# Performance work log

Hardware: AMD Instinct MI355X
Metric: run time of the kernel (lower is better)

Reference implementation:

```python
import jax, jax.numpy as jnp
import numpy as np

N, E, G = 50000, 400000, 512
F_IN, H = 128, 128  # OPS_LENGTH, hidden_channels
NEG_SLOPE = 0.2
BN_EPS = 1e-5


def seg_softmax(e, idx, n):
    m = jax.ops.segment_max(e, idx, num_segments=n)
    ex = jnp.exp(e - m[idx])
    s = jax.ops.segment_sum(ex, idx, num_segments=n)
    return ex / (s[idx] + 1e-16)


def gatv2(x, src, dst, Wl, Wr, att, b, n):
    # PyG GATv2Conv, heads=1: e = att . leaky_relu(Wl x_src + Wr x_dst),
    # alpha = softmax over incoming edges per dst, out = sum alpha * Wl x_src + b
    xl = x @ Wl
    xr = x @ Wr
    z = jax.nn.leaky_relu(xl[src] + xr[dst], NEG_SLOPE)  # [E, out]
    e = jnp.einsum('ed,d->e', z, att)
    a = seg_softmax(e, dst, n)
    return jax.ops.segment_sum(xl[src] * a[:, None], dst, num_segments=n) + b


def bn_eval(x, g, b, m, v):
    return (x - m) * jax.lax.rsqrt(v + BN_EPS) * g + b


def setup_inputs() -> dict:
    key = jax.random.key(0)
    ks = jax.random.split(key, 40)
    d = {}
    d['x'] = jax.random.normal(ks[0], (N, F_IN), dtype=jnp.float32)
    d['edge_index'] = jax.random.randint(ks[1], (2, E), 0, N)
    d['batch'] = jnp.sort(jax.random.randint(ks[2], (N,), 0, G))
    def lin(k, i, o, s=None):
        s = s if s is not None else 1.0 / np.sqrt(i)
        return jax.random.normal(k, (i, o), dtype=jnp.float32) * s
    # conv1: 128->128, conv2: 128->256, conv3: 256->128
    d['Wl1'] = lin(ks[3], F_IN, H); d['Wr1'] = lin(ks[4], F_IN, H)
    d['att1'] = jax.random.normal(ks[5], (H,), dtype=jnp.float32) * 0.1
    d['b1'] = jnp.zeros((H,), jnp.float32)
    d['Wl2'] = lin(ks[6], H, 2 * H); d['Wr2'] = lin(ks[7], H, 2 * H)
    d['att2'] = jax.random.normal(ks[8], (2 * H,), dtype=jnp.float32) * 0.1
    d['b2'] = jnp.zeros((2 * H,), jnp.float32)
    d['Wl3'] = lin(ks[9], 2 * H, H); d['Wr3'] = lin(ks[10], 2 * H, H)
    d['att3'] = jax.random.normal(ks[11], (H,), dtype=jnp.float32) * 0.1
    d['b3'] = jnp.zeros((H,), jnp.float32)
    d['Wlin1'] = lin(ks[12], H, 128); d['blin1'] = jnp.zeros((128,), jnp.float32)
    d['Wlin2'] = lin(ks[13], 128, 64); d['blin2'] = jnp.zeros((64,), jnp.float32)
    d['Wlin3'] = lin(ks[14], 64, 2); d['blin3'] = jnp.zeros((2,), jnp.float32)
    for name, dim, i in [('bng', H, 15), ('bn1', 128, 19), ('bn2', 64, 23)]:
        d[name + '_g'] = jax.random.uniform(ks[i], (dim,), minval=0.5, maxval=1.5)
        d[name + '_b'] = jax.random.normal(ks[i + 1], (dim,), dtype=jnp.float32) * 0.1
        d[name + '_m'] = jax.random.normal(ks[i + 2], (dim,), dtype=jnp.float32) * 0.1
        d[name + '_v'] = jax.random.uniform(ks[i + 3], (dim,), minval=0.5, maxval=1.5)
    return d


def reference(x, edge_index, batch, Wl1, Wr1, att1, b1, Wl2, Wr2, att2, b2,
              Wl3, Wr3, att3, b3, Wlin1, blin1, Wlin2, blin2, Wlin3, blin3,
              bng_g, bng_b, bng_m, bng_v, bn1_g, bn1_b, bn1_m, bn1_v,
              bn2_g, bn2_b, bn2_m, bn2_v):
    src, dst = edge_index[0], edge_index[1]
    h = jax.nn.relu(gatv2(x, src, dst, Wl1, Wr1, att1, b1, N))
    h = jax.nn.relu(gatv2(h, src, dst, Wl2, Wr2, att2, b2, N))
    h = gatv2(h, src, dst, Wl3, Wr3, att3, b3, N)
    # global_mean_pool
    sums = jax.ops.segment_sum(h, batch, num_segments=G)
    cnt = jax.ops.segment_sum(jnp.ones((N,), h.dtype), batch, num_segments=G)
    g = sums / jnp.maximum(cnt, 1.0)[:, None]
    # dropout p=0.5 is identity in eval mode; BatchNorms in eval mode
    g = bn_eval(g, bng_g, bng_b, bng_m, bng_v)
    g = bn_eval(jax.nn.relu(g @ Wlin1 + blin1), bn1_g, bn1_b, bn1_m, bn1_v)
    g = bn_eval(jax.nn.relu(g @ Wlin2 + blin2), bn2_g, bn2_b, bn2_m, bn2_v)
    return jax.nn.relu(g @ Wlin3 + blin3)
```

## Files before the change

### kernel.cpp

```cpp
#include <hip/hip_runtime.h>
#include <math.h>

#define N_NODES 50000
#define N_EDGES 400000
#define N_GRAPHS 512
#define NEG_SLOPE 0.2f
#define BN_EPS 1e-5f
#define SCAN_BLOCKS 49

#define C6 0.8656170245333781f
#define C4 0.5770780163555854f
#define THR_LOG2 11.541560327111708f

typedef __attribute__((ext_vector_type(8))) short bf16x8;
typedef __attribute__((ext_vector_type(4))) float f32x4;

__device__ __forceinline__ ushort f2b(float f) {
    unsigned u = __float_as_uint(f);
    unsigned r = (u + 0x7fffu + ((u >> 16) & 1u)) >> 16;
    return (ushort)r;
}
__device__ __forceinline__ float b2f(ushort u) {
    return __uint_as_float((unsigned)u << 16);
}

__global__ void cvt_kernel(const float* __restrict__ in, ushort* __restrict__ out,
                           int total4) {
    const int i = blockIdx.x * 256 + threadIdx.x;
    if (i >= total4) return;
    float4 v = *(const float4*)(in + (size_t)i * 4);
    ushort4 o;
    o.x = f2b(v.x); o.y = f2b(v.y); o.z = f2b(v.z); o.w = f2b(v.w);
    *(ushort4*)(out + (size_t)i * 4) = o;
}

__global__ void wcvt_all_kernel(const float* __restrict__ Wl1, const float* __restrict__ Wr1,
                                const float* __restrict__ Wl2, const float* __restrict__ Wr2,
                                const float* __restrict__ Wl3, const float* __restrict__ Wr3,
                                ushort* __restrict__ wt1, ushort* __restrict__ wt2,
                                ushort* __restrict__ wt3) {
    const int i = blockIdx.x * 256 + threadIdx.x;
    if (i < 32768) {
        const int m = i >> 7, k = i & 127;
        const float v = (m < 128) ? Wl1[k * 128 + m] : Wr1[k * 128 + (m - 128)];
        wt1[i] = f2b(v);
    } else if (i < 98304) {
        const int j = i - 32768;
        const int m = j >> 7, k = j & 127;
        const float v = (m < 256) ? Wl2[k * 256 + m] : Wr2[k * 256 + (m - 256)];
        wt2[j] = f2b(v);
    } else if (i < 163840) {
        const int j = i - 98304;
        const int m = j >> 8, k = j & 255;
        const float v = (m < 128) ? Wl3[k * 128 + m] : Wr3[k * 128 + (m - 128)];
        wt3[j] = f2b(v);
    }
}

__global__ __launch_bounds__(256) void gemm_bf16_kernel(
    const ushort* __restrict__ A, const ushort* __restrict__ Bt,
    ushort* __restrict__ Cl, float* __restrict__ Cr, int n, int K, int FO) {
    __shared__ ushort As[128][40];
    __shared__ ushort Bs[128][40];
    const int tid = threadIdx.x;
    const int row0 = blockIdx.x * 128;
    const int col0 = blockIdx.y * 128;
    const int w = tid >> 6, lane = tid & 63;
    const int wr = (w >> 1) * 64, wc = (w & 1) * 64;
    const int lr = lane & 15, kg = lane >> 4;

    const int srow = tid >> 1, shalf = tid & 1;

    f32x4 acc[4][4];
#pragma unroll
    for (int i = 0; i < 4; ++i)
#pragma unroll
        for (int j = 0; j < 4; ++j) acc[i][j] = (f32x4){0.f, 0.f, 0.f, 0.f};

    for (int k0 = 0; k0 < K; k0 += 32) {
        {
            const int gr = row0 + srow;
            uint4 v0 = make_uint4(0, 0, 0, 0), v1 = v0;
            if (gr < n) {
                const uint4* p = (const uint4*)(A + (size_t)gr * K + k0) + shalf * 2;
                v0 = p[0]; v1 = p[1];
            }
            uint4* d = (uint4*)&As[srow][shalf * 16];
            d[0] = v0; d[1] = v1;
            const int gb = col0 + srow;
            const uint4* p = (const uint4*)(Bt + (size_t)gb * K + k0) + shalf * 2;
            uint4* db = (uint4*)&Bs[srow][shalf * 16];
            db[0] = p[0]; db[1] = p[1];
        }
        __syncthreads();
        bf16x8 af[4], bfr[4];
#pragma unroll
        for (int mi = 0; mi < 4; ++mi)
            af[mi] = *(const bf16x8*)&As[wr + mi * 16 + lr][kg * 8];
#pragma unroll
        for (int ni = 0; ni < 4; ++ni)
            bfr[ni] = *(const bf16x8*)&Bs[wc + ni * 16 + lr][kg * 8];
#pragma unroll
        for (int mi = 0; mi < 4; ++mi)
#pragma unroll
            for (int ni = 0; ni < 4; ++ni)
                acc[mi][ni] = __builtin_amdgcn_mfma_f32_16x16x32_bf16(
                    af[mi], bfr[ni], acc[mi][ni], 0, 0, 0);
        __syncthreads();
    }
    const bool left = (col0 < FO);
    const int cbase = left ? col0 : col0 - FO;
#pragma unroll
    for (int mi = 0; mi < 4; ++mi)
#pragma unroll
        for (int ni = 0; ni < 4; ++ni)
#pragma unroll
            for (int j = 0; j < 4; ++j) {
                const int r = row0 + wr + mi * 16 + kg * 4 + j;
                if (r < n) {
                    const int c = cbase + wc + ni * 16 + lr;
                    if (left)
                        Cl[(size_t)r * FO + c] = f2b(acc[mi][ni][j]);
                    else
                        Cr[(size_t)r * FO + c] = acc[mi][ni][j];
                }
            }
}

__global__ void deg_count_kernel(const int* __restrict__ ei, int* __restrict__ deg) {
    const int e = blockIdx.x * 256 + threadIdx.x;
    if (e < N_EDGES) atomicAdd(&deg[ei[N_EDGES + e]], 1);
}

__global__ __launch_bounds__(256) void scanA_kernel(const int* __restrict__ deg,
                                                    int* __restrict__ rowp,
                                                    int* __restrict__ bsum) {
    const int t = threadIdx.x, b = blockIdx.x;
    const int i0 = b * 1024 + t * 4;
    int4 d = make_int4(0, 0, 0, 0);
    if (i0 + 3 < N_NODES) d = *(const int4*)(deg + i0);
    else {
        if (i0 + 0 < N_NODES) d.x = deg[i0 + 0];
        if (i0 + 1 < N_NODES) d.y = deg[i0 + 1];
        if (i0 + 2 < N_NODES) d.z = deg[i0 + 2];
    }
    const int tsum = d.x + d.y + d.z + d.w;
    int inc = tsum;
    const int lane = t & 63, wave = t >> 6;
#pragma unroll
    for (int o = 1; o < 64; o <<= 1) {
        int v = __shfl_up(inc, o, 64);
        if (lane >= o) inc += v;
    }
    __shared__ int wsum[4];
    if (lane == 63) wsum[wave] = inc;
    __syncthreads();
    int wbase = 0;
#pragma unroll
    for (int ww = 0; ww < 4; ++ww)
        if (ww < wave) wbase += wsum[ww];
    const int texcl = wbase + inc - tsum;
    int4 o4;
    o4.x = texcl;
    o4.y = o4.x + d.x;
    o4.z = o4.y + d.y;
    o4.w = o4.z + d.z;
    if (i0 + 3 < N_NODES) *(int4*)(rowp + i0) = o4;
    else {
        if (i0 + 0 < N_NODES) rowp[i0 + 0] = o4.x;
        if (i0 + 1 < N_NODES) rowp[i0 + 1] = o4.y;
        if (i0 + 2 < N_NODES) rowp[i0 + 2] = o4.z;
    }
    if (t == 255) bsum[b] = wbase + inc;
}

__global__ __launch_bounds__(256) void scanC_kernel(const int* __restrict__ bsum,
                                                    int* __restrict__ rowp) {
    const int t = threadIdx.x, b = blockIdx.x;
    __shared__ int base_s;
    if (t < 64) {
        int v = (t < b) ? bsum[t] : 0;
#pragma unroll
        for (int o = 32; o; o >>= 1) v += __shfl_xor(v, o, 64);
        if (t == 0) base_s = v;
    }
    __syncthreads();
    const int base = base_s;
    const int i0 = b * 1024 + t * 4;
    if (base != 0) {
        if (i0 + 3 < N_NODES) {
            int4 v = *(int4*)(rowp + i0);
            v.x += base; v.y += base; v.z += base; v.w += base;
            *(int4*)(rowp + i0) = v;
        } else {
            if (i0 + 0 < N_NODES) rowp[i0 + 0] += base;
            if (i0 + 1 < N_NODES) rowp[i0 + 1] += base;
            if (i0 + 2 < N_NODES) rowp[i0 + 2] += base;
        }
    }
    if (b == 0 && t == 0) rowp[N_NODES] = N_EDGES;
}

__global__ void csr_fill_kernel(const int* __restrict__ ei, const int* __restrict__ rowp,
                                int* __restrict__ cursor, int* __restrict__ csr_src) {
    const int e = blockIdx.x * 256 + threadIdx.x;
    if (e >= N_EDGES) return;
    const int d = ei[N_EDGES + e];
    const int pos = atomicAdd(&cursor[d], 1);
    csr_src[rowp[d] + pos] = ei[e];
}

template <int VEC>
__device__ __forceinline__ void sm_upd(float& m, float& s, float* acc, float p,
                                       const float* l) {
    if (p > m + THR_LOG2) {
        const float sc = __builtin_amdgcn_exp2f(m - p);
        s = s * sc + 1.f;
#pragma unroll
        for (int k = 0; k < VEC; ++k) acc[k] = acc[k] * sc + l[k];
        m = p;
    } else {
        const float w = __builtin_amdgcn_exp2f(p - m);
        s += w;
#pragma unroll
        for (int k = 0; k < VEC; ++k) acc[k] += w * l[k];
    }
}

template <int FO, int VEC>
__global__ __launch_bounds__(256) void gat_edge_kernel(
    const int* __restrict__ rowp, const int* __restrict__ csr_src,
    const ushort* __restrict__ xlb, const float* __restrict__ xr,
    const float* __restrict__ att, const float* __restrict__ bias,
    float* __restrict__ outf, ushort* __restrict__ outb, int do_relu) {
    const int d = blockIdx.x * 4 + (threadIdx.x >> 6);
    const int lane = threadIdx.x & 63;
    if (d >= N_NODES) return;
    const int co = lane * VEC;

    float a6[VEC], a4[VEC], r[VEC];
    if constexpr (VEC == 4) {
        float4 t4 = *(const float4*)(att + co);
        a6[0] = C6 * t4.x; a6[1] = C6 * t4.y; a6[2] = C6 * t4.z; a6[3] = C6 * t4.w;
        a4[0] = C4 * t4.x; a4[1] = C4 * t4.y; a4[2] = C4 * t4.z; a4[3] = C4 * t4.w;
        t4 = *(const float4*)(xr + (size_t)d * FO + co);
        r[0] = t4.x; r[1] = t4.y; r[2] = t4.z; r[3] = t4.w;
    } else {
        float2 t2 = *(const float2*)(att + co);
        a6[0] = C6 * t2.x; a6[1] = C6 * t2.y;
        a4[0] = C4 * t2.x; a4[1] = C4 * t2.y;
        t2 = *(const float2*)(xr + (size_t)d * FO + co);
        r[0] = t2.x; r[1] = t2.y;
    }

    const int jb = rowp[d], je = rowp[d + 1];
    float m0 = -INFINITY, s0 = 0.f, m1 = -INFINITY, s1 = 0.f;
    float acc0[VEC] = {}, acc1[VEC] = {};

    int j = jb;
    for (; j + 1 < je; j += 2) {
        const int src0 = csr_src[j];
        const int src1 = csr_src[j + 1];
        float l0[VEC], l1[VEC];
        if constexpr (VEC == 4) {
            ushort4 t0 = *(const ushort4*)(xlb + (size_t)src0 * FO + co);
            ushort4 t1 = *(const ushort4*)(xlb + (size_t)src1 * FO + co);
            l0[0] = b2f(t0.x); l0[1] = b2f(t0.y); l0[2] = b2f(t0.z); l0[3] = b2f(t0.w);
            l1[0] = b2f(t1.x); l1[1] = b2f(t1.y); l1[2] = b2f(t1.z); l1[3] = b2f(t1.w);
        } else {
            ushort2 t0 = *(const ushort2*)(xlb + (size_t)src0 * FO + co);
            ushort2 t1 = *(const ushort2*)(xlb + (size_t)src1 * FO + co);
            l0[0] = b2f(t0.x); l0[1] = b2f(t0.y);
            l1[0] = b2f(t1.x); l1[1] = b2f(t1.y);
        }
        float p0 = 0.f, p1 = 0.f;
#pragma unroll
        for (int k = 0; k < VEC; ++k) {
            const float z0 = l0[k] + r[k];
            const float z1 = l1[k] + r[k];
            p0 = fmaf(a6[k], z0, p0); p0 = fmaf(a4[k], fabsf(z0), p0);
            p1 = fmaf(a6[k], z1, p1); p1 = fmaf(a4[k], fabsf(z1), p1);
        }
#pragma unroll
        for (int o = 32; o; o >>= 1) {
            p0 += __shfl_xor(p0, o, 64);
            p1 += __shfl_xor(p1, o, 64);
        }
        sm_upd<VEC>(m0, s0, acc0, p0, l0);
        sm_upd<VEC>(m1, s1, acc1, p1, l1);
    }
    if (j < je) {
        const int src0 = csr_src[j];
        float l0[VEC];
        if constexpr (VEC == 4) {
            ushort4 t0 = *(const ushort4*)(xlb + (size_t)src0 * FO + co);
            l0[0] = b2f(t0.x); l0[1] = b2f(t0.y); l0[2] = b2f(t0.z); l0[3] = b2f(t0.w);
        } else {
            ushort2 t0 = *(const ushort2*)(xlb + (size_t)src0 * FO + co);
            l0[0] = b2f(t0.x); l0[1] = b2f(t0.y);
        }
        float p0 = 0.f;
#pragma unroll
        for (int k = 0; k < VEC; ++k) {
            const float z0 = l0[k] + r[k];
            p0 = fmaf(a6[k], z0, p0); p0 = fmaf(a4[k], fabsf(z0), p0);
        }
#pragma unroll
        for (int o = 32; o; o >>= 1) p0 += __shfl_xor(p0, o, 64);
        sm_upd<VEC>(m0, s0, acc0, p0, l0);
    }

    float s, acc[VEC];
    if (je > jb) {
        const float M = fmaxf(m0, m1);
        const float sc0 = __builtin_amdgcn_exp2f(m0 - M);
        const float sc1 = __builtin_amdgcn_exp2f(m1 - M);
        s = s0 * sc0 + s1 * sc1;
#pragma unroll
        for (int k = 0; k < VEC; ++k) acc[k] = acc0[k] * sc0 + acc1[k] * sc1;
    } else {
        s = 0.f;
#pragma unroll
        for (int k = 0; k < VEC; ++k) acc[k] = 0.f;
    }

    const float inv = 1.f / (s + 1e-16f);
#pragma unroll
    for (int k = 0; k < VEC; ++k) {
        float v = acc[k] * inv + bias[co + k];
        if (do_relu) v = fmaxf(v, 0.f);
        acc[k] = v;
    }
    if (outf) {
        if constexpr (VEC == 4)
            *(float4*)(outf + (size_t)d * FO + co) = make_float4(acc[0], acc[1], acc[2], acc[3]);
        else
            *(float2*)(outf + (size_t)d * FO + co) = make_float2(acc[0], acc[1]);
    }
    if (outb) {
        if constexpr (VEC == 4) {
            ushort4 o; o.x = f2b(acc[0]); o.y = f2b(acc[1]); o.z = f2b(acc[2]); o.w = f2b(acc[3]);
            *(ushort4*)(outb + (size_t)d * FO + co) = o;
        } else {
            ushort2 o; o.x = f2b(acc[0]); o.y = f2b(acc[1]);
            *(ushort2*)(outb + (size_t)d * FO + co) = o;
        }
    }
}

__global__ void gstart_kernel(const int* __restrict__ batch, int* __restrict__ gstart) {
    const int i = blockIdx.x * 256 + threadIdx.x;
    if (i >= N_NODES) return;
    const int b = batch[i];
    if (i == 0) {
        for (int g = 0; g <= b; ++g) gstart[g] = 0;
    } else {
        const int pb = batch[i - 1];
        for (int g = pb + 1; g <= b; ++g) gstart[g] = i;
    }
    if (i == N_NODES - 1) {
        for (int g = b + 1; g <= N_GRAPHS; ++g) gstart[g] = N_NODES;
    }
}

__global__ __launch_bounds__(128) void pool2_kernel(const float* __restrict__ h,
                                                    const int* __restrict__ gstart,
                                                    float* __restrict__ gsum,
                                                    float* __restrict__ gcnt) {
    const int g = blockIdx.x, t = threadIdx.x;
    const int b = gstart[g], e = gstart[g + 1];
    float s = 0.f;
    for (int i = b; i < e; ++i) s += h[(size_t)i * 128 + t];
    gsum[g * 128 + t] = s;
    if (t == 0) gcnt[g] = (float)(e - b);
}

__global__ __launch_bounds__(128) void mlp_kernel(
    const float* __restrict__ gsum, const float* __restrict__ gcnt,
    const float* __restrict__ W1, const float* __restrict__ b1,
    const float* __restrict__ W2, const float* __restrict__ b2,
    const float* __restrict__ W3, const float* __restrict__ b3,
    const float* __restrict__ bng_g, const float* __restrict__ bng_b,
    const float* __restrict__ bng_m, const float* __restrict__ bng_v,
    const float* __restrict__ bn1_g, const float* __restrict__ bn1_b,
    const float* __restrict__ bn1_m, const float* __restrict__ bn1_v,
    const float* __restrict__ bn2_g, const float* __restrict__ bn2_b,
    const float* __restrict__ bn2_m, const float* __restrict__ bn2_v,
    float* __restrict__ out) {
    __shared__ float s0[128], s1[128], s2[64];
    const int g = blockIdx.x, t = threadIdx.x;
    const float cnt = fmaxf(gcnt[g], 1.f);
    float v = gsum[g * 128 + t] / cnt;
    v = (v - bng_m[t]) * rsqrtf(bng_v[t] + BN_EPS) * bng_g[t] + bng_b[t];
    s0[t] = v;
    __syncthreads();
    float a1 = b1[t];
    for (int i = 0; i < 128; ++i) a1 += s0[i] * W1[i * 128 + t];
    a1 = fmaxf(a1, 0.f);
    a1 = (a1 - bn1_m[t]) * rsqrtf(bn1_v[t] + BN_EPS) * bn1_g[t] + bn1_b[t];
    s1[t] = a1;
    __syncthreads();
    if (t < 64) {
        float a2 = b2[t];
        for (int i = 0; i < 128; ++i) a2 += s1[i] * W2[i * 64 + t];
        a2 = fmaxf(a2, 0.f);
        a2 = (a2 - bn2_m[t]) * rsqrtf(bn2_v[t] + BN_EPS) * bn2_g[t] + bn2_b[t];
        s2[t] = a2;
    }
    __syncthreads();
    if (t < 2) {
        float a3 = b3[t];
        for (int i = 0; i < 64; ++i) a3 += s2[i] * W3[i * 2 + t];
        out[g * 2 + t] = fmaxf(a3, 0.f);
    }
}

extern "C" void kernel_launch(void* const* d_in, const int* in_sizes, int n_in,
                              void* d_out, int out_size, void* d_ws, size_t ws_size,
                              hipStream_t stream) {
    const float* x = (const float*)d_in[0];
    const int* ei = (const int*)d_in[1];
    const int* batch = (const int*)d_in[2];
    const float* Wl1 = (const float*)d_in[3];
    const float* Wr1 = (const float*)d_in[4];
    const float* att1 = (const float*)d_in[5];
    const float* b1 = (const float*)d_in[6];
    const float* Wl2 = (const float*)d_in[7];
    const float* Wr2 = (const float*)d_in[8];
    const float* att2 = (const float*)d_in[9];
    const float* b2 = (const float*)d_in[10];
    const float* Wl3 = (const float*)d_in[11];
    const float* Wr3 = (const float*)d_in[12];
    const float* att3 = (const float*)d_in[13];
    const float* b3 = (const float*)d_in[14];
    const float* Wlin1 = (const float*)d_in[15];
    const float* blin1 = (const float*)d_in[16];
    const float* Wlin2 = (const float*)d_in[17];
    const float* blin2 = (const float*)d_in[18];
    const float* Wlin3 = (const float*)d_in[19];
    const float* blin3 = (const float*)d_in[20];
    const float* bng_g = (const float*)d_in[21];
    const float* bng_b = (const float*)d_in[22];
    const float* bng_m = (const float*)d_in[23];
    const float* bng_v = (const float*)d_in[24];
    const float* bn1_g = (const float*)d_in[25];
    const float* bn1_b = (const float*)d_in[26];
    const float* bn1_m = (const float*)d_in[27];
    const float* bn1_v = (const float*)d_in[28];
    const float* bn2_g = (const float*)d_in[29];
    const float* bn2_b = (const float*)d_in[30];
    const float* bn2_m = (const float*)d_in[31];
    const float* bn2_v = (const float*)d_in[32];

    float* ws = (float*)d_ws;
    ushort* xlb = (ushort*)ws;
    float* xr = (float*)(xlb + (size_t)N_NODES * 256);
    float* h3 = xr + (size_t)N_NODES * 256;
    ushort* hbf = (ushort*)(h3 + (size_t)N_NODES * 128);
    ushort* wt1 = hbf + (size_t)N_NODES * 256;
    ushort* wt2 = wt1 + 256 * 128;
    ushort* wt3 = wt2 + 512 * 128;
    int* deg = (int*)(wt3 + 256 * 256);
    int* cursor = deg + N_NODES;
    int* rowp = cursor + N_NODES;
    int* csr_src = rowp + N_NODES + 1;
    int* gstart = csr_src + N_EDGES;
    int* bsum = gstart + N_GRAPHS + 1;
    float* gsum = (float*)(bsum + SCAN_BLOCKS);
    float* gcnt = gsum + (size_t)N_GRAPHS * 128;

    const int eb = (N_EDGES + 255) / 256;

    hipMemsetAsync(deg, 0, (size_t)N_NODES * 2 * 4, stream);
    deg_count_kernel<<<eb, 256, 0, stream>>>(ei, deg);
    scanA_kernel<<<SCAN_BLOCKS, 256, 0, stream>>>(deg, rowp, bsum);
    scanC_kernel<<<SCAN_BLOCKS, 256, 0, stream>>>(bsum, rowp);
    csr_fill_kernel<<<eb, 256, 0, stream>>>(ei, rowp, cursor, csr_src);
    gstart_kernel<<<(N_NODES + 255) / 256, 256, 0, stream>>>(batch, gstart);

    wcvt_all_kernel<<<640, 256, 0, stream>>>(Wl1, Wr1, Wl2, Wr2, Wl3, Wr3, wt1, wt2, wt3);
    cvt_kernel<<<(N_NODES * 128 / 4 + 255) / 256, 256, 0, stream>>>(
        x, hbf, N_NODES * 128 / 4);

    const int nb = (N_NODES + 3) / 4;
    const int gx = (N_NODES + 127) / 128;

    gemm_bf16_kernel<<<dim3(gx, 2), 256, 0, stream>>>(hbf, wt1, xlb, xr, N_NODES, 128, 128);
    gat_edge_kernel<128, 2><<<nb, 256, 0, stream>>>(rowp, csr_src, xlb, xr,
                                                    att1, b1, nullptr, hbf, 1);
    gemm_bf16_kernel<<<dim3(gx, 4), 256, 0, stream>>>(hbf, wt2, xlb, xr, N_NODES, 128, 256);
    gat_edge_kernel<256, 4><<<nb, 256, 0, stream>>>(rowp, csr_src, xlb, xr,
                                                    att2, b2, nullptr, hbf, 1);
    gemm_bf16_kernel<<<dim3(gx, 2), 256, 0, stream>>>(hbf, wt3, xlb, xr, N_NODES, 256, 128);
    gat_edge_kernel<128, 2><<<nb, 256, 0, stream>>>(rowp, csr_src, xlb, xr,
                                                    att3, b3, h3, nullptr, 0);

    pool2_kernel<<<N_GRAPHS, 128, 0, stream>>>(h3, gstart, gsum, gcnt);

    mlp_kernel<<<N_GRAPHS, 128, 0, stream>>>(
        gsum, gcnt, Wlin1, blin1, Wlin2, blin2, Wlin3, blin3,
        bng_g, bng_b, bng_m, bng_v, bn1_g, bn1_b, bn1_m, bn1_v,
        bn2_g, bn2_b, bn2_m, bn2_v, (float*)d_out);
}
```

Before: 317.3 us.

## Store xl and xr interleaved in bf16 and unroll edge loop by four

The GEMM now writes one interleaved bf16 buffer in which each row holds the xl half followed by the xr half, replacing the separate bf16 xl and fp32 xr arrays. This halves the bytes written for xr and read per destination node. The GAT edge kernel keeps four independent online-softmax accumulators instead of two, giving four gathers in flight per iteration. The costs are reduced precision of xr, a larger row stride for the gathered xl rows that lowers cache density, and more register pressure from the extra accumulators.

```diff
diff --git a/kernel.cpp b/kernel.cpp
--- a/kernel.cpp
+++ b/kernel.cpp
@@ -59,7 +59,7 @@
 
 __global__ __launch_bounds__(256) void gemm_bf16_kernel(
     const ushort* __restrict__ A, const ushort* __restrict__ Bt,
-    ushort* __restrict__ Cl, float* __restrict__ Cr, int n, int K, int FO) {
+    ushort* __restrict__ C, int n, int K, int M) {
     __shared__ ushort As[128][40];
     __shared__ ushort Bs[128][40];
     const int tid = threadIdx.x;
@@ -108,8 +108,6 @@
                     af[mi], bfr[ni], acc[mi][ni], 0, 0, 0);
         __syncthreads();
     }
-    const bool left = (col0 < FO);
-    const int cbase = left ? col0 : col0 - FO;
 #pragma unroll
     for (int mi = 0; mi < 4; ++mi)
 #pragma unroll
@@ -117,13 +115,8 @@
 #pragma unroll
             for (int j = 0; j < 4; ++j) {
                 const int r = row0 + wr + mi * 16 + kg * 4 + j;
-                if (r < n) {
-                    const int c = cbase + wc + ni * 16 + lr;
-                    if (left)
-                        Cl[(size_t)r * FO + c] = f2b(acc[mi][ni][j]);
-                    else
-                        Cr[(size_t)r * FO + c] = acc[mi][ni][j];
-                }
+                if (r < n)
+                    C[(size_t)r * M + col0 + wc + ni * 16 + lr] = f2b(acc[mi][ni][j]);
             }
 }
 
@@ -230,7 +223,7 @@
 template <int FO, int VEC>
 __global__ __launch_bounds__(256) void gat_edge_kernel(
     const int* __restrict__ rowp, const int* __restrict__ csr_src,
-    const ushort* __restrict__ xlb, const float* __restrict__ xr,
+    const ushort* __restrict__ hx,
     const float* __restrict__ att, const float* __restrict__ bias,
     float* __restrict__ outf, ushort* __restrict__ outb, int do_relu) {
     const int d = blockIdx.x * 4 + (threadIdx.x >> 6);
@@ -243,106 +236,110 @@
         float4 t4 = *(const float4*)(att + co);
         a6[0] = C6 * t4.x; a6[1] = C6 * t4.y; a6[2] = C6 * t4.z; a6[3] = C6 * t4.w;
         a4[0] = C4 * t4.x; a4[1] = C4 * t4.y; a4[2] = C4 * t4.z; a4[3] = C4 * t4.w;
-        t4 = *(const float4*)(xr + (size_t)d * FO + co);
-        r[0] = t4.x; r[1] = t4.y; r[2] = t4.z; r[3] = t4.w;
+        ushort4 u4 = *(const ushort4*)(hx + (size_t)d * (2 * FO) + FO + co);
+        r[0] = b2f(u4.x); r[1] = b2f(u4.y); r[2] = b2f(u4.z); r[3] = b2f(u4.w);
     } else {
         float2 t2 = *(const float2*)(att + co);
         a6[0] = C6 * t2.x; a6[1] = C6 * t2.y;
         a4[0] = C4 * t2.x; a4[1] = C4 * t2.y;
-        t2 = *(const float2*)(xr + (size_t)d * FO + co);
-        r[0] = t2.x; r[1] = t2.y;
+        ushort2 u2 = *(const ushort2*)(hx + (size_t)d * (2 * FO) + FO + co);
+        r[0] = b2f(u2.x); r[1] = b2f(u2.y);
     }
 
     const int jb = rowp[d], je = rowp[d + 1];
-    float m0 = -INFINITY, s0 = 0.f, m1 = -INFINITY, s1 = 0.f;
-    float acc0[VEC] = {}, acc1[VEC] = {};
+    float ms[4] = {-INFINITY, -INFINITY, -INFINITY, -INFINITY};
+    float ss[4] = {0.f, 0.f, 0.f, 0.f};
+    float acc[4][VEC] = {};
 
     int j = jb;
-    for (; j + 1 < je; j += 2) {
-        const int src0 = csr_src[j];
-        const int src1 = csr_src[j + 1];
-        float l0[VEC], l1[VEC];
-        if constexpr (VEC == 4) {
-            ushort4 t0 = *(const ushort4*)(xlb + (size_t)src0 * FO + co);
-            ushort4 t1 = *(const ushort4*)(xlb + (size_t)src1 * FO + co);
-            l0[0] = b2f(t0.x); l0[1] = b2f(t0.y); l0[2] = b2f(t0.z); l0[3] = b2f(t0.w);
-            l1[0] = b2f(t1.x); l1[1] = b2f(t1.y); l1[2] = b2f(t1.z); l1[3] = b2f(t1.w);
-        } else {
-            ushort2 t0 = *(const ushort2*)(xlb + (size_t)src0 * FO + co);
-            ushort2 t1 = *(const ushort2*)(xlb + (size_t)src1 * FO + co);
-            l0[0] = b2f(t0.x); l0[1] = b2f(t0.y);
-            l1[0] = b2f(t1.x); l1[1] = b2f(t1.y);
-        }
-        float p0 = 0.f, p1 = 0.f;
-#pragma unroll
-        for (int k = 0; k < VEC; ++k) {
-            const float z0 = l0[k] + r[k];
-            const float z1 = l1[k] + r[k];
-            p0 = fmaf(a6[k], z0, p0); p0 = fmaf(a4[k], fabsf(z0), p0);
-            p1 = fmaf(a6[k], z1, p1); p1 = fmaf(a4[k], fabsf(z1), p1);
+    for (; j + 3 < je; j += 4) {
+        int src[4];
+#pragma unroll
+        for (int q = 0; q < 4; ++q) src[q] = csr_src[j + q];
+        float l[4][VEC];
+        float p[4] = {0.f, 0.f, 0.f, 0.f};
+#pragma unroll
+        for (int q = 0; q < 4; ++q) {
+            if constexpr (VEC == 4) {
+                ushort4 t = *(const ushort4*)(hx + (size_t)src[q] * (2 * FO) + co);
+                l[q][0] = b2f(t.x); l[q][1] = b2f(t.y); l[q][2] = b2f(t.z); l[q][3] = b2f(t.w);
+            } else {
+                ushort2 t = *(const ushort2*)(hx + (size_t)src[q] * (2 * FO) + co);
+                l[q][0] = b2f(t.x); l[q][1] = b2f(t.y);
+            }
+#pragma unroll
+            for (int k = 0; k < VEC; ++k) {
+                const float z = l[q][k] + r[k];
+                p[q] = fmaf(a6[k], z, p[q]);
+                p[q] = fmaf(a4[k], fabsf(z), p[q]);
+            }
         }
 #pragma unroll
         for (int o = 32; o; o >>= 1) {
-            p0 += __shfl_xor(p0, o, 64);
-            p1 += __shfl_xor(p1, o, 64);
-        }
-        sm_upd<VEC>(m0, s0, acc0, p0, l0);
-        sm_upd<VEC>(m1, s1, acc1, p1, l1);
-    }
-    if (j < je) {
+#pragma unroll
+            for (int q = 0; q < 4; ++q) p[q] += __shfl_xor(p[q], o, 64);
+        }
+#pragma unroll
+        for (int q = 0; q < 4; ++q) sm_upd<VEC>(ms[q], ss[q], acc[q], p[q], l[q]);
+    }
+    for (int q = 0; j < je; ++j, ++q) {
         const int src0 = csr_src[j];
         float l0[VEC];
         if constexpr (VEC == 4) {
-            ushort4 t0 = *(const ushort4*)(xlb + (size_t)src0 * FO + co);
-            l0[0] = b2f(t0.x); l0[1] = b2f(t0.y); l0[2] = b2f(t0.z); l0[3] = b2f(t0.w);
+            ushort4 t = *(const ushort4*)(hx + (size_t)src0 * (2 * FO) + co);
+            l0[0] = b2f(t.x); l0[1] = b2f(t.y); l0[2] = b2f(t.z); l0[3] = b2f(t.w);
         } else {
-            ushort2 t0 = *(const ushort2*)(xlb + (size_t)src0 * FO + co);
-            l0[0] = b2f(t0.x); l0[1] = b2f(t0.y);
+            ushort2 t = *(const ushort2*)(hx + (size_t)src0 * (2 * FO) + co);
+            l0[0] = b2f(t.x); l0[1] = b2f(t.y);
         }
         float p0 = 0.f;
 #pragma unroll
         for (int k = 0; k < VEC; ++k) {
-            const float z0 = l0[k] + r[k];
-            p0 = fmaf(a6[k], z0, p0); p0 = fmaf(a4[k], fabsf(z0), p0);
+            const float z = l0[k] + r[k];
+            p0 = fmaf(a6[k], z, p0);
+            p0 = fmaf(a4[k], fabsf(z), p0);
         }
 #pragma unroll
         for (int o = 32; o; o >>= 1) p0 += __shfl_xor(p0, o, 64);
-        sm_upd<VEC>(m0, s0, acc0, p0, l0);
-    }
-
-    float s, acc[VEC];
+        sm_upd<VEC>(ms[q], ss[q], acc[q], p0, l0);
+    }
+
+    float s, accm[VEC];
     if (je > jb) {
-        const float M = fmaxf(m0, m1);
-        const float sc0 = __builtin_amdgcn_exp2f(m0 - M);
-        const float sc1 = __builtin_amdgcn_exp2f(m1 - M);
-        s = s0 * sc0 + s1 * sc1;
-#pragma unroll
-        for (int k = 0; k < VEC; ++k) acc[k] = acc0[k] * sc0 + acc1[k] * sc1;
+        const float M = fmaxf(fmaxf(ms[0], ms[1]), fmaxf(ms[2], ms[3]));
+        float sc[4];
+#pragma unroll
+        for (int q = 0; q < 4; ++q) sc[q] = __builtin_amdgcn_exp2f(ms[q] - M);
+        s = ss[0] * sc[0] + ss[1] * sc[1] + ss[2] * sc[2] + ss[3] * sc[3];
+#pragma unroll
+        for (int k = 0; k < VEC; ++k)
+            accm[k] = acc[0][k] * sc[0] + acc[1][k] * sc[1] +
+                      acc[2][k] * sc[2] + acc[3][k] * sc[3];
     } else {
         s = 0.f;
 #pragma unroll
-        for (int k = 0; k < VEC; ++k) acc[k] = 0.f;
+        for (int k = 0; k < VEC; ++k) accm[k] = 0.f;
     }
 
     const float inv = 1.f / (s + 1e-16f);
 #pragma unroll
     for (int k = 0; k < VEC; ++k) {
-        float v = acc[k] * inv + bias[co + k];
+        float v = accm[k] * inv + bias[co + k];
         if (do_relu) v = fmaxf(v, 0.f);
-        acc[k] = v;
+        accm[k] = v;
     }
     if (outf) {
         if constexpr (VEC == 4)
-            *(float4*)(outf + (size_t)d * FO + co) = make_float4(acc[0], acc[1], acc[2], acc[3]);
+            *(float4*)(outf + (size_t)d * FO + co) = make_float4(accm[0], accm[1], accm[2], accm[3]);
         else
-            *(float2*)(outf + (size_t)d * FO + co) = make_float2(acc[0], acc[1]);
+            *(float2*)(outf + (size_t)d * FO + co) = make_float2(accm[0], accm[1]);
     }
     if (outb) {
         if constexpr (VEC == 4) {
-            ushort4 o; o.x = f2b(acc[0]); o.y = f2b(acc[1]); o.z = f2b(acc[2]); o.w = f2b(acc[3]);
+            ushort4 o; o.x = f2b(accm[0]); o.y = f2b(accm[1]); o.z = f2b(accm[2]); o.w = f2b(accm[3]);
             *(ushort4*)(outb + (size_t)d * FO + co) = o;
         } else {
-            ushort2 o; o.x = f2b(acc[0]); o.y = f2b(acc[1]);
+            ushort2 o; o.x = f2b(accm[0]); o.y = f2b(accm[1]);
             *(ushort2*)(outb + (size_t)d * FO + co) = o;
         }
     }
@@ -453,9 +450,8 @@
     const float* bn2_v = (const float*)d_in[32];
 
     float* ws = (float*)d_ws;
-    ushort* xlb = (ushort*)ws;
-    float* xr = (float*)(xlb + (size_t)N_NODES * 256);
-    float* h3 = xr + (size_t)N_NODES * 256;
+    ushort* hx = (ushort*)ws;
+    float* h3 = (float*)(hx + (size_t)N_NODES * 512);
     ushort* hbf = (ushort*)(h3 + (size_t)N_NODES * 128);
     ushort* wt1 = hbf + (size_t)N_NODES * 256;
     ushort* wt2 = wt1 + 256 * 128;
@@ -485,14 +481,14 @@
     const int nb = (N_NODES + 3) / 4;
     const int gx = (N_NODES + 127) / 128;
 
-    gemm_bf16_kernel<<<dim3(gx, 2), 256, 0, stream>>>(hbf, wt1, xlb, xr, N_NODES, 128, 128);
-    gat_edge_kernel<128, 2><<<nb, 256, 0, stream>>>(rowp, csr_src, xlb, xr,
+    gemm_bf16_kernel<<<dim3(gx, 2), 256, 0, stream>>>(hbf, wt1, hx, N_NODES, 128, 256);
+    gat_edge_kernel<128, 2><<<nb, 256, 0, stream>>>(rowp, csr_src, hx,
                                                     att1, b1, nullptr, hbf, 1);
-    gemm_bf16_kernel<<<dim3(gx, 4), 256, 0, stream>>>(hbf, wt2, xlb, xr, N_NODES, 128, 256);
-    gat_edge_kernel<256, 4><<<nb, 256, 0, stream>>>(rowp, csr_src, xlb, xr,
+    gemm_bf16_kernel<<<dim3(gx, 4), 256, 0, stream>>>(hbf, wt2, hx, N_NODES, 128, 512);
+    gat_edge_kernel<256, 4><<<nb, 256, 0, stream>>>(rowp, csr_src, hx,
                                                     att2, b2, nullptr, hbf, 1);
-    gemm_bf16_kernel<<<dim3(gx, 2), 256, 0, stream>>>(hbf, wt3, xlb, xr, N_NODES, 256, 128);
-    gat_edge_kernel<128, 2><<<nb, 256, 0, stream>>>(rowp, csr_src, xlb, xr,
+    gemm_bf16_kernel<<<dim3(gx, 2), 256, 0, stream>>>(hbf, wt3, hx, N_NODES, 256, 256);
+    gat_edge_kernel<128, 2><<<nb, 256, 0, stream>>>(rowp, csr_src, hx,
                                                     att3, b3, h3, nullptr, 0);
 
     pool2_kernel<<<N_GRAPHS, 128, 0, stream>>>(h3, gstart, gsum, gcnt);
```

New measurement: 365.4 us. 1.15x slower.
